# Kernel optimization log

Hardware: AMD Instinct MI355X
Metric: run time of the kernel (lower is better)

## Reference

```python
import jax, jax.numpy as jnp
import numpy as np

# BTT factorization dims: d_in = m1*m2 = 4096, d_out = n1*n2 = 4096, rs = (1, R, 1)
B = 4096
M1 = 64
M2 = 64
N1 = 64
N2 = 64
R = 4  # tt_rank


def setup_inputs() -> dict:
    key = jax.random.key(0)
    kx, k1, k2 = jax.random.split(key, 3)
    # xavier_normal_(W, gain=1/sqrt(fan_in_factor)); fan_in/out of xavier use last two dims
    std1 = (1.0 / (M1 * 1) ** 0.5) * (2.0 / (M1 * 1 + N1 * R)) ** 0.5
    std2 = (1.0 / (M2 * R) ** 0.5) * (2.0 / (M2 * R + N2 * 1)) ** 0.5
    x = jax.random.normal(kx, (B, M1 * M2), dtype=jnp.float32)
    W1 = jax.random.normal(k1, (M2, M1 * 1, N1 * R), dtype=jnp.float32) * std1
    W2 = jax.random.normal(k2, (N1, M2 * R, N2 * 1), dtype=jnp.float32) * std2
    return {"x": x, "W1": W1, "W2": W2}


def reference(x, W1, W2):
    b = x.shape[0]
    # stage 1: contract m1, batched over m2 -> intermediate (b, m2, n1, r2)
    xr = x.reshape(b, M2, M1)                             # (b, m2, m1)
    t = jnp.einsum('bma,mac->bmc', xr, W1)                # (b, m2, n1*r2)
    t = t.reshape(b, M2, N1, R)                           # (b, m2, n1, r2)
    # stage 2: contract (m2, r2), batched over n1 -> (b, n1, n2)
    t = t.transpose(0, 2, 1, 3).reshape(b, N1, M2 * R)    # (b, n1, m2*r2)
    y = jnp.einsum('bnd,ndo->bno', t, W2)                 # (b, n1, n2)
    return y.reshape(b, N1 * N2)
```

## Files before the change

### kernel.cpp

```cpp
#include <hip/hip_runtime.h>

typedef unsigned short u16;
typedef unsigned int u32;
typedef __attribute__((ext_vector_type(8))) short short8;
typedef __attribute__((ext_vector_type(4))) float f32x4;

__device__ __forceinline__ u16 f2bf(float f) {
    union { float f; u32 u; } c; c.f = f;
    u32 u = c.u;
    return (u16)((u + 0x7fffu + ((u >> 16) & 1u)) >> 16);
}

#define MFMA16(A, B, C) __builtin_amdgcn_mfma_f32_16x16x32_bf16((A), (B), (C), 0, 0, 0)

__global__ __launch_bounds__(256) void prep_all(const float* __restrict__ x,
                                                const float* __restrict__ W1,
                                                const float* __restrict__ W2,
                                                u16* __restrict__ W1F,
                                                u16* __restrict__ W2F,
                                                u16* __restrict__ XF) {
    __shared__ u16 sh[16384];
    const int bid = blockIdx.x;
    const int t = threadIdx.x;

    if (bid < 4096) {
        const int bt = bid >> 6, m2 = bid & 63;
        const int r = t >> 2, lr = r & 15, bl = r >> 4;
        const int c0 = (t & 3) * 16;
        const float* src = x + ((size_t)bt * 64 + r) * 4096 + m2 * 64 + c0;
        float4 f[4];
        #pragma unroll
        for (int s = 0; s < 4; ++s) f[s] = ((const float4*)src)[s];
        u16 v[16];
        #pragma unroll
        for (int s = 0; s < 4; ++s) {
            v[s * 4 + 0] = f2bf(f[s].x); v[s * 4 + 1] = f2bf(f[s].y);
            v[s * 4 + 2] = f2bf(f[s].z); v[s * 4 + 3] = f2bf(f[s].w);
        }
        #pragma unroll
        for (int h = 0; h < 2; ++h) {
            int cc = (t & 3) * 2 + h;
            int ks = cc >> 2, q = cc & 3;
            int off = (((bl * 2 + ks) * 4 + q) << 7) + lr * 8;
            short8 pk;
            #pragma unroll
            for (int j = 0; j < 8; ++j) pk[j] = (short)v[h * 8 + j];
            *(short8*)(&sh[off]) = pk;
        }
        __syncthreads();
        u16* dst = XF + (size_t)bid * 4096 + t * 16;
        *(short8*)(dst) = *(const short8*)(&sh[t * 16]);
        *(short8*)(dst + 8) = *(const short8*)(&sh[t * 16 + 8]);
    } else if (bid < 4160) {
        const int m2 = bid - 4096;
        const float* src = W1 + (size_t)m2 * 16384 + t * 64;
        #pragma unroll
        for (int s = 0; s < 16; ++s) {
            float4 f = ((const float4*)src)[s];
            float fv[4] = {f.x, f.y, f.z, f.w};
            #pragma unroll
            for (int e = 0; e < 4; ++e) {
                int elem = t * 64 + s * 4 + e;
                int m1 = elem >> 8, c = elem & 255;
                int nb = c >> 5, ct = (c >> 4) & 1, lr = c & 15;
                int ks = m1 >> 5, q = (m1 >> 3) & 3, j = m1 & 7;
                sh[(((((nb * 2 + ct) * 2 + ks) * 4 + q)) << 7) + lr * 8 + j] =
                    f2bf(fv[e]);
            }
        }
        __syncthreads();
        u16* dst = W1F + (size_t)m2 * 16384 + t * 64;
        #pragma unroll
        for (int s = 0; s < 8; ++s)
            *(short8*)(dst + s * 8) = *(const short8*)(&sh[t * 64 + s * 8]);
    } else {
        const int n1 = bid - 4160;
        const float* src = W2 + (size_t)n1 * 16384 + t * 64;
        #pragma unroll
        for (int s = 0; s < 16; ++s) {
            float4 f = ((const float4*)src)[s];
            float fv[4] = {f.x, f.y, f.z, f.w};
            #pragma unroll
            for (int e = 0; e < 4; ++e) {
                int elem = t * 64 + s * 4 + e;
                int k = elem >> 6, n2 = elem & 63;
                int m2b = k >> 5, q = (k >> 3) & 3, j = k & 7;
                int nt = n2 >> 4, lr = n2 & 15;
                sh[((((m2b * 4 + nt) * 4 + q)) << 7) + lr * 8 + j] = f2bf(fv[e]);
            }
        }
        __syncthreads();
        u16* dst = W2F + (size_t)n1 * 16384 + t * 64;
        #pragma unroll
        for (int s = 0; s < 8; ++s)
            *(short8*)(dst + s * 8) = *(const short8*)(&sh[t * 64 + s * 8]);
    }
}

__global__ __launch_bounds__(512) void btt_main(const u16* __restrict__ XF,
                                                const u16* __restrict__ W1F,
                                                const u16* __restrict__ W2F,
                                                float* __restrict__ out) {
    __shared__ u16 t_lds[64 * 260];

    const int tid = threadIdx.x;
    const int w = tid >> 6;
    const int lane = tid & 63;
    const int q = lane >> 4;
    const int lr = lane & 15;
    const int bt = blockIdx.x & 63;
    const int nb = blockIdx.x >> 6;
    const int n1 = nb * 8 + w;

    const f32x4 fz = {0.f, 0.f, 0.f, 0.f};
    f32x4 acc2[4][4];
    #pragma unroll
    for (int i = 0; i < 4; ++i)
        #pragma unroll
        for (int j = 0; j < 4; ++j) acc2[i][j] = fz;

    for (int m2b = 0; m2b < 8; ++m2b) {
        const int m2 = m2b * 8 + w;

        short8 a1[2][2];
        {
            const u16* p = W1F + ((size_t)m2 * 8 + nb) * 2048 + lane * 8;
            #pragma unroll
            for (int ct = 0; ct < 2; ++ct)
                #pragma unroll
                for (int ks = 0; ks < 2; ++ks)
                    a1[ct][ks] = *(const short8*)(p + (ct * 2 + ks) * 512);
        }
        short8 b1[4][2];
        {
            const u16* p = XF + ((size_t)bt * 64 + m2) * 4096 + lane * 8;
            #pragma unroll
            for (int bl = 0; bl < 4; ++bl)
                #pragma unroll
                for (int ks = 0; ks < 2; ++ks)
                    b1[bl][ks] = *(const short8*)(p + (bl * 2 + ks) * 512);
        }
        f32x4 acc1[2][4];
        #pragma unroll
        for (int ct = 0; ct < 2; ++ct)
            #pragma unroll
            for (int bl = 0; bl < 4; ++bl) acc1[ct][bl] = fz;
        #pragma unroll
        for (int ks = 0; ks < 2; ++ks)
            #pragma unroll
            for (int ct = 0; ct < 2; ++ct)
                #pragma unroll
                for (int bl = 0; bl < 4; ++bl)
                    acc1[ct][bl] = MFMA16(a1[ct][ks], b1[bl][ks], acc1[ct][bl]);

        __syncthreads();

        #pragma unroll
        for (int ct = 0; ct < 2; ++ct)
            #pragma unroll
            for (int bl = 0; bl < 4; ++bl) {
                int off = (bl * 16 + lr) * 260 + w * 32 + ct * 16 + q * 4;
                u32 lo = (u32)f2bf(acc1[ct][bl][0]) | ((u32)f2bf(acc1[ct][bl][1]) << 16);
                u32 hi = (u32)f2bf(acc1[ct][bl][2]) | ((u32)f2bf(acc1[ct][bl][3]) << 16);
                *(uint2*)(&t_lds[off]) = make_uint2(lo, hi);
            }

        __syncthreads();

        short8 a2[4];
        #pragma unroll
        for (int bl = 0; bl < 4; ++bl) {
            int base = (bl * 16 + lr) * 260 + (2 * q) * 32 + w * 4;
            union { short8 v; uint2 u[2]; } tmp;
            tmp.u[0] = *(const uint2*)(&t_lds[base]);
            tmp.u[1] = *(const uint2*)(&t_lds[base + 32]);
            a2[bl] = tmp.v;
        }
        short8 b2[4];
        {
            const u16* p = W2F + (size_t)n1 * 16384 + m2b * 2048 + lane * 8;
            #pragma unroll
            for (int nt = 0; nt < 4; ++nt)
                b2[nt] = *(const short8*)(p + nt * 512);
        }
        #pragma unroll
        for (int bl = 0; bl < 4; ++bl)
            #pragma unroll
            for (int nt = 0; nt < 4; ++nt)
                acc2[bl][nt] = MFMA16(a2[bl], b2[nt], acc2[bl][nt]);
    }

    #pragma unroll
    for (int bl = 0; bl < 4; ++bl)
        #pragma unroll
        for (int nt = 0; nt < 4; ++nt)
            #pragma unroll
            for (int g = 0; g < 4; ++g) {
                long row = bt * 64 + bl * 16 + q * 4 + g;
                long col = (long)n1 * 64 + nt * 16 + lr;
                out[row * 4096 + col] = acc2[bl][nt][g];
            }
}

__global__ __launch_bounds__(512) void btt_nows(const float* __restrict__ x,
                                                const float* __restrict__ W1,
                                                const float* __restrict__ W2,
                                                float* __restrict__ out) {
    __shared__ u16 t_lds[64 * 260];
    const int tid = threadIdx.x;
    const int w = tid >> 6;
    const int lane = tid & 63;
    const int q = lane >> 4;
    const int lr = lane & 15;
    const int bt = blockIdx.x & 63;
    const int nb = blockIdx.x >> 6;
    const int n1 = nb * 8 + w;

    const f32x4 fz = {0.f, 0.f, 0.f, 0.f};
    f32x4 acc2[4][4];
    #pragma unroll
    for (int i = 0; i < 4; ++i)
        #pragma unroll
        for (int j = 0; j < 4; ++j) acc2[i][j] = fz;

    for (int m2b = 0; m2b < 8; ++m2b) {
        const int m2 = m2b * 8 + w;
        short8 ax[4][2];
        #pragma unroll
        for (int bl = 0; bl < 4; ++bl)
            #pragma unroll
            for (int ks = 0; ks < 2; ++ks) {
                const float* p = x + (size_t)(bt * 64 + bl * 16 + lr) * 4096 +
                                 m2 * 64 + ks * 32 + q * 8;
                float4 ua = *(const float4*)(p);
                float4 ub = *(const float4*)(p + 4);
                short8 r;
                r[0] = (short)f2bf(ua.x); r[1] = (short)f2bf(ua.y);
                r[2] = (short)f2bf(ua.z); r[3] = (short)f2bf(ua.w);
                r[4] = (short)f2bf(ub.x); r[5] = (short)f2bf(ub.y);
                r[6] = (short)f2bf(ub.z); r[7] = (short)f2bf(ub.w);
                ax[bl][ks] = r;
            }
        short8 bw1[2][2];
        #pragma unroll
        for (int ct = 0; ct < 2; ++ct)
            #pragma unroll
            for (int ks = 0; ks < 2; ++ks)
                #pragma unroll
                for (int j = 0; j < 8; ++j)
                    bw1[ct][ks][j] = (short)f2bf(W1[m2 * 16384 +
                                                    (ks * 32 + q * 8 + j) * 256 +
                                                    nb * 32 + ct * 16 + lr]);
        f32x4 acc1[4][2];
        #pragma unroll
        for (int bl = 0; bl < 4; ++bl)
            #pragma unroll
            for (int ct = 0; ct < 2; ++ct) acc1[bl][ct] = fz;
        #pragma unroll
        for (int ks = 0; ks < 2; ++ks)
            #pragma unroll
            for (int bl = 0; bl < 4; ++bl)
                #pragma unroll
                for (int ct = 0; ct < 2; ++ct)
                    acc1[bl][ct] = MFMA16(ax[bl][ks], bw1[ct][ks], acc1[bl][ct]);

        __syncthreads();
        #pragma unroll
        for (int bl = 0; bl < 4; ++bl)
            #pragma unroll
            for (int ct = 0; ct < 2; ++ct)
                #pragma unroll
                for (int g = 0; g < 4; ++g)
                    t_lds[(bl * 16 + q * 4 + g) * 260 + w * 32 + ct * 16 + lr] =
                        f2bf(acc1[bl][ct][g]);
        __syncthreads();

        short8 a2[4];
        #pragma unroll
        for (int bl = 0; bl < 4; ++bl) {
            int base = (bl * 16 + lr) * 260 + (2 * q) * 32 + w * 4;
            union { short8 v; uint2 u[2]; } tmp;
            tmp.u[0] = *(const uint2*)(&t_lds[base]);
            tmp.u[1] = *(const uint2*)(&t_lds[base + 32]);
            a2[bl] = tmp.v;
        }
        short8 b2[4];
        #pragma unroll
        for (int nt = 0; nt < 4; ++nt)
            #pragma unroll
            for (int j = 0; j < 8; ++j)
                b2[nt][j] = (short)f2bf(W2[n1 * 16384 +
                                           (m2b * 32 + q * 8 + j) * 64 +
                                           nt * 16 + lr]);
        #pragma unroll
        for (int bl = 0; bl < 4; ++bl)
            #pragma unroll
            for (int nt = 0; nt < 4; ++nt)
                acc2[bl][nt] = MFMA16(a2[bl], b2[nt], acc2[bl][nt]);
    }

    #pragma unroll
    for (int bl = 0; bl < 4; ++bl)
        #pragma unroll
        for (int nt = 0; nt < 4; ++nt)
            #pragma unroll
            for (int g = 0; g < 4; ++g) {
                long row = bt * 64 + bl * 16 + q * 4 + g;
                long col = (long)n1 * 64 + nt * 16 + lr;
                out[row * 4096 + col] = acc2[bl][nt][g];
            }
}

extern "C" void kernel_launch(void* const* d_in, const int* in_sizes, int n_in,
                              void* d_out, int out_size, void* d_ws, size_t ws_size,
                              hipStream_t stream) {
    const float* x  = (const float*)d_in[0];
    const float* W1 = (const float*)d_in[1];
    const float* W2 = (const float*)d_in[2];
    float* out = (float*)d_out;

    const size_t N_W1F = (size_t)64 * 16384;
    const size_t N_W2F = (size_t)64 * 16384;
    const size_t N_XF  = (size_t)4096 * 4096;
    const size_t WS_NEED = (N_W1F + N_W2F + N_XF) * sizeof(u16);

    if (ws_size >= WS_NEED) {
        u16* W1F = (u16*)d_ws;
        u16* W2F = W1F + N_W1F;
        u16* XF  = W2F + N_W2F;
        prep_all<<<4096 + 64 + 64, 256, 0, stream>>>(x, W1, W2, W1F, W2F, XF);
        btt_main<<<512, 512, 0, stream>>>(XF, W1F, W2F, out);
    } else {
        btt_nows<<<512, 512, 0, stream>>>(x, W1, W2, out);
    }
}
```

Measured before the change: 165.2 us.

## Fuse x bf16 conversion into main kernel and halve batch tile

Drops the separate pass that converted x to a swizzled bf16 workspace. The main kernel now loads fp32 x directly from global memory and converts it in registers before the first MFMA stage. The batch tile shrinks from 64 to 32 rows, doubling the grid to 1024 blocks, and the weight-prep kernel now uses coalesced float4 loads. This removes a 32 MB bf16 write and re-read, but every block re-reads fp32 x rows, so x traffic across the n1 blocks doubles in bytes and W1F/W2F reuse per block is lower.

```diff
diff --git a/kernel.cpp b/kernel.cpp
--- a/kernel.cpp
+++ b/kernel.cpp
@@ -13,54 +13,24 @@
 
 #define MFMA16(A, B, C) __builtin_amdgcn_mfma_f32_16x16x32_bf16((A), (B), (C), 0, 0, 0)
 
-__global__ __launch_bounds__(256) void prep_all(const float* __restrict__ x,
-                                                const float* __restrict__ W1,
-                                                const float* __restrict__ W2,
-                                                u16* __restrict__ W1F,
-                                                u16* __restrict__ W2F,
-                                                u16* __restrict__ XF) {
+__global__ __launch_bounds__(256) void prep_w(const float* __restrict__ W1,
+                                              const float* __restrict__ W2,
+                                              u16* __restrict__ W1F,
+                                              u16* __restrict__ W2F) {
     __shared__ u16 sh[16384];
     const int bid = blockIdx.x;
     const int t = threadIdx.x;
 
-    if (bid < 4096) {
-        const int bt = bid >> 6, m2 = bid & 63;
-        const int r = t >> 2, lr = r & 15, bl = r >> 4;
-        const int c0 = (t & 3) * 16;
-        const float* src = x + ((size_t)bt * 64 + r) * 4096 + m2 * 64 + c0;
-        float4 f[4];
-        #pragma unroll
-        for (int s = 0; s < 4; ++s) f[s] = ((const float4*)src)[s];
-        u16 v[16];
-        #pragma unroll
-        for (int s = 0; s < 4; ++s) {
-            v[s * 4 + 0] = f2bf(f[s].x); v[s * 4 + 1] = f2bf(f[s].y);
-            v[s * 4 + 2] = f2bf(f[s].z); v[s * 4 + 3] = f2bf(f[s].w);
-        }
-        #pragma unroll
-        for (int h = 0; h < 2; ++h) {
-            int cc = (t & 3) * 2 + h;
-            int ks = cc >> 2, q = cc & 3;
-            int off = (((bl * 2 + ks) * 4 + q) << 7) + lr * 8;
-            short8 pk;
-            #pragma unroll
-            for (int j = 0; j < 8; ++j) pk[j] = (short)v[h * 8 + j];
-            *(short8*)(&sh[off]) = pk;
-        }
-        __syncthreads();
-        u16* dst = XF + (size_t)bid * 4096 + t * 16;
-        *(short8*)(dst) = *(const short8*)(&sh[t * 16]);
-        *(short8*)(dst + 8) = *(const short8*)(&sh[t * 16 + 8]);
-    } else if (bid < 4160) {
-        const int m2 = bid - 4096;
-        const float* src = W1 + (size_t)m2 * 16384 + t * 64;
+    if (bid < 64) {
+        const int m2 = bid;
+        const float4* src = (const float4*)(W1 + (size_t)m2 * 16384);
         #pragma unroll
         for (int s = 0; s < 16; ++s) {
-            float4 f = ((const float4*)src)[s];
+            float4 f = src[s * 256 + t];
             float fv[4] = {f.x, f.y, f.z, f.w};
             #pragma unroll
             for (int e = 0; e < 4; ++e) {
-                int elem = t * 64 + s * 4 + e;
+                int elem = (s * 256 + t) * 4 + e;
                 int m1 = elem >> 8, c = elem & 255;
                 int nb = c >> 5, ct = (c >> 4) & 1, lr = c & 15;
                 int ks = m1 >> 5, q = (m1 >> 3) & 3, j = m1 & 7;
@@ -74,15 +44,15 @@
         for (int s = 0; s < 8; ++s)
             *(short8*)(dst + s * 8) = *(const short8*)(&sh[t * 64 + s * 8]);
     } else {
-        const int n1 = bid - 4160;
-        const float* src = W2 + (size_t)n1 * 16384 + t * 64;
+        const int n1 = bid - 64;
+        const float4* src = (const float4*)(W2 + (size_t)n1 * 16384);
         #pragma unroll
         for (int s = 0; s < 16; ++s) {
-            float4 f = ((const float4*)src)[s];
+            float4 f = src[s * 256 + t];
             float fv[4] = {f.x, f.y, f.z, f.w};
             #pragma unroll
             for (int e = 0; e < 4; ++e) {
-                int elem = t * 64 + s * 4 + e;
+                int elem = (s * 256 + t) * 4 + e;
                 int k = elem >> 6, n2 = elem & 63;
                 int m2b = k >> 5, q = (k >> 3) & 3, j = k & 7;
                 int nt = n2 >> 4, lr = n2 & 15;
@@ -97,25 +67,25 @@
     }
 }
 
-__global__ __launch_bounds__(512) void btt_main(const u16* __restrict__ XF,
-                                                const u16* __restrict__ W1F,
-                                                const u16* __restrict__ W2F,
-                                                float* __restrict__ out) {
-    __shared__ u16 t_lds[64 * 260];
+__global__ __launch_bounds__(512) void btt_fused(const float* __restrict__ x,
+                                                 const u16* __restrict__ W1F,
+                                                 const u16* __restrict__ W2F,
+                                                 float* __restrict__ out) {
+    __shared__ u16 t_lds[32 * 260];
 
     const int tid = threadIdx.x;
     const int w = tid >> 6;
     const int lane = tid & 63;
     const int q = lane >> 4;
     const int lr = lane & 15;
-    const int bt = blockIdx.x & 63;
-    const int nb = blockIdx.x >> 6;
+    const int bt = blockIdx.x & 127;
+    const int nb = blockIdx.x >> 7;
     const int n1 = nb * 8 + w;
 
     const f32x4 fz = {0.f, 0.f, 0.f, 0.f};
-    f32x4 acc2[4][4];
+    f32x4 acc2[2][4];
     #pragma unroll
-    for (int i = 0; i < 4; ++i)
+    for (int i = 0; i < 2; ++i)
         #pragma unroll
         for (int j = 0; j < 4; ++j) acc2[i][j] = fz;
 
@@ -131,34 +101,49 @@
                 for (int ks = 0; ks < 2; ++ks)
                     a1[ct][ks] = *(const short8*)(p + (ct * 2 + ks) * 512);
         }
-        short8 b1[4][2];
+        short8 b2[4];
         {
-            const u16* p = XF + ((size_t)bt * 64 + m2) * 4096 + lane * 8;
-            #pragma unroll
-            for (int bl = 0; bl < 4; ++bl)
-                #pragma unroll
-                for (int ks = 0; ks < 2; ++ks)
-                    b1[bl][ks] = *(const short8*)(p + (bl * 2 + ks) * 512);
-        }
-        f32x4 acc1[2][4];
+            const u16* p = W2F + (size_t)n1 * 16384 + m2b * 2048 + lane * 8;
+            #pragma unroll
+            for (int nt = 0; nt < 4; ++nt)
+                b2[nt] = *(const short8*)(p + nt * 512);
+        }
+        short8 bx[2][2];
+        #pragma unroll
+        for (int bl = 0; bl < 2; ++bl)
+            #pragma unroll
+            for (int ks = 0; ks < 2; ++ks) {
+                const float* p = x + (size_t)(bt * 32 + bl * 16 + lr) * 4096 +
+                                 m2 * 64 + ks * 32 + q * 8;
+                float4 ua = *(const float4*)(p);
+                float4 ub = *(const float4*)(p + 4);
+                short8 r;
+                r[0] = (short)f2bf(ua.x); r[1] = (short)f2bf(ua.y);
+                r[2] = (short)f2bf(ua.z); r[3] = (short)f2bf(ua.w);
+                r[4] = (short)f2bf(ub.x); r[5] = (short)f2bf(ub.y);
+                r[6] = (short)f2bf(ub.z); r[7] = (short)f2bf(ub.w);
+                bx[bl][ks] = r;
+            }
+
+        f32x4 acc1[2][2];
         #pragma unroll
         for (int ct = 0; ct < 2; ++ct)
             #pragma unroll
-            for (int bl = 0; bl < 4; ++bl) acc1[ct][bl] = fz;
+            for (int bl = 0; bl < 2; ++bl) acc1[ct][bl] = fz;
         #pragma unroll
         for (int ks = 0; ks < 2; ++ks)
             #pragma unroll
             for (int ct = 0; ct < 2; ++ct)
                 #pragma unroll
-                for (int bl = 0; bl < 4; ++bl)
-                    acc1[ct][bl] = MFMA16(a1[ct][ks], b1[bl][ks], acc1[ct][bl]);
+                for (int bl = 0; bl < 2; ++bl)
+                    acc1[ct][bl] = MFMA16(a1[ct][ks], bx[bl][ks], acc1[ct][bl]);
 
         __syncthreads();
 
         #pragma unroll
         for (int ct = 0; ct < 2; ++ct)
             #pragma unroll
-            for (int bl = 0; bl < 4; ++bl) {
+            for (int bl = 0; bl < 2; ++bl) {
                 int off = (bl * 16 + lr) * 260 + w * 32 + ct * 16 + q * 4;
                 u32 lo = (u32)f2bf(acc1[ct][bl][0]) | ((u32)f2bf(acc1[ct][bl][1]) << 16);
                 u32 hi = (u32)f2bf(acc1[ct][bl][2]) | ((u32)f2bf(acc1[ct][bl][3]) << 16);
@@ -167,36 +152,29 @@
 
         __syncthreads();
 
-        short8 a2[4];
-        #pragma unroll
-        for (int bl = 0; bl < 4; ++bl) {
+        short8 a2[2];
+        #pragma unroll
+        for (int bl = 0; bl < 2; ++bl) {
             int base = (bl * 16 + lr) * 260 + (2 * q) * 32 + w * 4;
             union { short8 v; uint2 u[2]; } tmp;
             tmp.u[0] = *(const uint2*)(&t_lds[base]);
             tmp.u[1] = *(const uint2*)(&t_lds[base + 32]);
             a2[bl] = tmp.v;
         }
-        short8 b2[4];
-        {
-            const u16* p = W2F + (size_t)n1 * 16384 + m2b * 2048 + lane * 8;
-            #pragma unroll
-            for (int nt = 0; nt < 4; ++nt)
-                b2[nt] = *(const short8*)(p + nt * 512);
-        }
-        #pragma unroll
-        for (int bl = 0; bl < 4; ++bl)
+        #pragma unroll
+        for (int bl = 0; bl < 2; ++bl)
             #pragma unroll
             for (int nt = 0; nt < 4; ++nt)
                 acc2[bl][nt] = MFMA16(a2[bl], b2[nt], acc2[bl][nt]);
     }
 
     #pragma unroll
-    for (int bl = 0; bl < 4; ++bl)
+    for (int bl = 0; bl < 2; ++bl)
         #pragma unroll
         for (int nt = 0; nt < 4; ++nt)
             #pragma unroll
             for (int g = 0; g < 4; ++g) {
-                long row = bt * 64 + bl * 16 + q * 4 + g;
+                long row = bt * 32 + bl * 16 + q * 4 + g;
                 long col = (long)n1 * 64 + nt * 16 + lr;
                 out[row * 4096 + col] = acc2[bl][nt][g];
             }
@@ -321,15 +299,13 @@
 
     const size_t N_W1F = (size_t)64 * 16384;
     const size_t N_W2F = (size_t)64 * 16384;
-    const size_t N_XF  = (size_t)4096 * 4096;
-    const size_t WS_NEED = (N_W1F + N_W2F + N_XF) * sizeof(u16);
+    const size_t WS_NEED = (N_W1F + N_W2F) * sizeof(u16);
 
     if (ws_size >= WS_NEED) {
         u16* W1F = (u16*)d_ws;
         u16* W2F = W1F + N_W1F;
-        u16* XF  = W2F + N_W2F;
-        prep_all<<<4096 + 64 + 64, 256, 0, stream>>>(x, W1, W2, W1F, W2F, XF);
-        btt_main<<<512, 512, 0, stream>>>(XF, W1F, W2F, out);
+        prep_w<<<128, 256, 0, stream>>>(W1, W2, W1F, W2F);
+        btt_fused<<<1024, 512, 0, stream>>>(x, W1F, W2F, out);
     } else {
         btt_nows<<<512, 512, 0, stream>>>(x, W1, W2, out);
     }
```

Measured after the change: 191.3 us. 15.7% more time.
